# Optimization experiments

Hardware: AMD Instinct MI355X
Metric: run time of the kernel (lower is better)

## Reference

```python
import jax, jax.numpy as jnp
import numpy as np

N_NODES = 50000
N_EDGES = 800000
N_GRAPHS = 64
IN_CH = 128
HID = 128
PROC_X = 128
Q_DIM = 768
PROC_Q = 128
OUT_CH = 32


def setup_inputs() -> dict:
    key = jax.random.key(0)
    ks = jax.random.split(key, 16)
    inp = {
        "x": jax.random.normal(ks[0], (N_NODES, IN_CH), dtype=jnp.float32),
        "edge_index": jax.random.randint(ks[1], (2, N_EDGES), 0, N_NODES, dtype=jnp.int64),
        "batch": jnp.sort(jax.random.randint(ks[2], (N_NODES,), 0, N_GRAPHS, dtype=jnp.int64)),
        "question_embedding": jax.random.normal(ks[3], (N_GRAPHS, Q_DIM), dtype=jnp.float32),
    }
    s = 1.0 / np.sqrt(HID)
    inp["W0"] = jax.random.uniform(ks[4], (IN_CH, HID), minval=-s, maxval=s)
    inp["b0"] = jnp.zeros((HID,), jnp.float32)
    inp["W1"] = jax.random.uniform(ks[5], (HID, HID), minval=-s, maxval=s)
    inp["b1"] = jnp.zeros((HID,), jnp.float32)
    inp["W2"] = jax.random.uniform(ks[6], (HID, PROC_X), minval=-s, maxval=s)
    inp["b2"] = jnp.zeros((PROC_X,), jnp.float32)
    inp["fc0_w"] = jax.random.uniform(ks[7], (Q_DIM, PROC_Q), minval=-s, maxval=s)
    inp["fc0_b"] = jnp.zeros((PROC_Q,), jnp.float32)
    inp["fc1_w"] = jax.random.uniform(ks[8], (PROC_X + PROC_Q, HID), minval=-s, maxval=s)
    inp["fc1_b"] = jnp.zeros((HID,), jnp.float32)
    inp["fc2_w"] = jax.random.uniform(ks[9], (HID, OUT_CH), minval=-s, maxval=s)
    inp["fc2_b"] = jnp.zeros((OUT_CH,), jnp.float32)
    return inp


def _gcn_norm(edge_index, n_nodes):
    """Add self-loops and compute symmetric GCN normalization per edge."""
    loop = jnp.arange(n_nodes, dtype=edge_index.dtype)
    src = jnp.concatenate([edge_index[0], loop])
    dst = jnp.concatenate([edge_index[1], loop])
    ones = jnp.ones_like(dst, dtype=jnp.float32)
    deg = jax.ops.segment_sum(ones, dst, num_segments=n_nodes)
    dinv = jnp.where(deg > 0, jax.lax.rsqrt(deg), 0.0)
    norm = dinv[src] * dinv[dst]  # [E+N]
    return src, dst, norm


def _gcn_conv(x, src, dst, norm, W, b):
    h = x @ W                                # [N, F_out]
    msg = h[src] * norm[:, None]             # gather + scale  [E+N, F_out]
    agg = jax.ops.segment_sum(msg, dst, num_segments=x.shape[0])
    return agg + b


def reference(x, edge_index, batch, question_embedding,
              W0, b0, W1, b1, W2, b2,
              fc0_w, fc0_b, fc1_w, fc1_b, fc2_w, fc2_b):
    n = x.shape[0]
    src, dst, norm = _gcn_norm(edge_index, n)
    h = jax.nn.relu(_gcn_conv(x, src, dst, norm, W0, b0))
    h = jax.nn.relu(_gcn_conv(h, src, dst, norm, W1, b1))
    h = jax.nn.relu(_gcn_conv(h, src, dst, norm, W2, b2))
    q = jax.nn.relu(question_embedding @ fc0_w + fc0_b)  # [G, PROC_Q]
    q_exp = q[batch]                                      # [N, PROC_Q]
    combined = jnp.concatenate([h, q_exp], axis=1)
    out = jax.nn.relu(combined @ fc1_w + fc1_b)
    out = out @ fc2_w + fc2_b
    return out
```

## Files before the change

### kernel.cpp

```cpp
#include <hip/hip_runtime.h>
#include <hip/hip_bf16.h>

#define N_NODES 50000
#define N_EDGES 800000
#define N_GRAPHS 64
#define LSTR 136
#define NP 50016

typedef __attribute__((ext_vector_type(4))) short s4v;
typedef __attribute__((ext_vector_type(8))) short s8v;
typedef __attribute__((ext_vector_type(16))) float f16v;

struct HL { short hi, lo; };

__device__ inline HL bsplit(float f) {
    HL r;
    unsigned u = __float_as_uint(f);
    unsigned rh = (u + 0x7FFFu + ((u >> 16) & 1u)) >> 16;
    r.hi = (short)rh;
    float fh = __uint_as_float(rh << 16);
    float fl = f - fh;
    unsigned u2 = __float_as_uint(fl);
    unsigned rl = (u2 + 0x7FFFu + ((u2 >> 16) & 1u)) >> 16;
    r.lo = (short)rl;
    return r;
}

__device__ inline unsigned short f2bf(float f) {
    unsigned u = __float_as_uint(f);
    return (unsigned short)((u + 0x7FFFu + ((u >> 16) & 1u)) >> 16);
}

__device__ inline float bflo(unsigned u) { return __uint_as_float(u << 16); }
__device__ inline float bfhi(unsigned u) { return __uint_as_float(u & 0xFFFF0000u); }


__global__ __launch_bounds__(512) void k_scan_a(const int* __restrict__ cnt8,
                                                int* __restrict__ rowptr,
                                                int* __restrict__ bsum,
                                                float* __restrict__ dinv,
                                                int* __restrict__ base8, int n) {
    __shared__ int s[512];
    int t = threadIdx.x;
    int i = blockIdx.x * 512 + t;
    int deg = 0;
    if (i < n) {
        int b = 0;
        #pragma unroll
        for (int p = 0; p < 8; ++p) {
            int c = cnt8[p * NP + i];
            base8[p * NP + i] = b;
            b += c;
        }
        deg = b;
        dinv[i] = rsqrtf((float)(deg + 1));
    }
    int pv = (deg + 7) & ~7;
    s[t] = pv;
    __syncthreads();
    for (int d = 1; d < 512; d <<= 1) {
        int x = (t >= d) ? s[t - d] : 0;
        __syncthreads();
        s[t] += x;
        __syncthreads();
    }
    if (i < n) rowptr[i] = s[t] - pv;
    if (t == 511) bsum[blockIdx.x] = s[511];
}

__global__ __launch_bounds__(512) void k_scan_c(int* __restrict__ rowptr,
                                                const int* __restrict__ bsum,
                                                int n, int nb) {
    __shared__ int sb[128];
    int t = threadIdx.x;
    if (t < 128) sb[t] = (t < nb) ? bsum[t] : 0;
    __syncthreads();
    for (int d = 1; d < 128; d <<= 1) {
        int x = 0;
        if (t < 128 && t >= d) x = sb[t - d];
        __syncthreads();
        if (t < 128) sb[t] += x;
        __syncthreads();
    }
    int add = (blockIdx.x > 0) ? sb[blockIdx.x - 1] : 0;
    int i = blockIdx.x * 512 + t;
    if (i < n) rowptr[i] += add;
    if (i == 0) rowptr[n] = sb[nb - 1];
}

__global__ __launch_bounds__(512) void k_prep(const float* __restrict__ qe,
                                              const float* __restrict__ fc0w,
                                              const float* __restrict__ fc0b,
                                              const float* __restrict__ fc1w,
                                              const float* __restrict__ fc1b,
                                              const float* __restrict__ W0,
                                              const float* __restrict__ W1,
                                              const float* __restrict__ W2,
                                              const float* __restrict__ fc2w,
                                              const int* __restrict__ ei,
                                              int* __restrict__ cnt8,
                                              int* __restrict__ rank,
                                              short* __restrict__ WH,
                                              short* __restrict__ WL,
                                              unsigned* __restrict__ Hsd,
                                              unsigned short* __restrict__ colA,
                                              float* __restrict__ qq, int E) {
    int b = blockIdx.x, tid = threadIdx.x;
    if (b >= 482) {
        int e = (b - 482) * 512 + tid;
        if (e < E) {
            int dst = ei[E + e];
            int p = b & 7;
            int r = atomicAdd(&cnt8[p * NP + dst], 1);
            rank[e] = (p << 24) | r;
        }
        return;
    }
    if (b == 481) {
        if (tid < 64) Hsd[(unsigned)N_NODES * 64u + tid] = 0u;
        if (tid >= 64 && tid < 128) Hsd[100001u * 64u + (unsigned)(tid - 64)] = 0u;
        return;
    }
    if (b >= 200) {
        int idx = (b - 200) * 512 + tid;
        if (idx < 143752) {
            uint4 p;
            p.x = p.y = p.z = p.w = 0xC350C350u;
            ((uint4*)colA)[idx] = p;
        }
        return;
    }
    if (b >= 64) {
        int i = (b - 64) * 512 + tid;
        float val;
        int dst;
        if (i < 65536) {
            int mat = i >> 14, off = i & 16383;
            int k = off >> 7, n = off & 127;
            const float* src = (mat == 0) ? W0 : (mat == 1) ? W1 : (mat == 2) ? W2 : fc1w;
            val = src[k * 128 + n];
            dst = mat * 16384 + n * 128 + k;
        } else {
            int off = i - 65536;
            int k = off >> 5, n = off & 31;
            val = fc2w[k * 32 + n];
            dst = 65536 + n * 128 + k;
        }
        HL r = bsplit(val);
        WH[dst] = r.hi;
        WL[dst] = r.lo;
        return;
    }
    __shared__ float qs[768];
    __shared__ float red[512];
    __shared__ float ql[128];
    const float* fc1bot = fc1w + 128 * 128;
    int g = b;
    for (int i = tid; i < 768; i += 512) qs[i] = qe[g * 768 + i];
    __syncthreads();
    int j = tid & 127, sl = tid >> 7;
    int kb = sl * 192;
    float a0 = 0, a1 = 0, a2 = 0, a3 = 0;
    for (int k = 0; k < 192; k += 4) {
        a0 += qs[kb + k + 0] * fc0w[(kb + k + 0) * 128 + j];
        a1 += qs[kb + k + 1] * fc0w[(kb + k + 1) * 128 + j];
        a2 += qs[kb + k + 2] * fc0w[(kb + k + 2) * 128 + j];
        a3 += qs[kb + k + 3] * fc0w[(kb + k + 3) * 128 + j];
    }
    red[tid] = (a0 + a1) + (a2 + a3);
    __syncthreads();
    if (tid < 128)
        ql[tid] = fmaxf(((red[tid] + red[tid + 128]) + (red[tid + 256] + red[tid + 384]))
                        + fc0b[tid], 0.f);
    __syncthreads();
    kb = sl * 32;
    float b0 = 0, b1 = 0;
    for (int k = 0; k < 32; k += 2) {
        b0 += ql[kb + k + 0] * fc1bot[(kb + k + 0) * 128 + j];
        b1 += ql[kb + k + 1] * fc1bot[(kb + k + 1) * 128 + j];
    }
    red[tid] = b0 + b1;
    __syncthreads();
    if (tid < 128)
        qq[g * 128 + tid] = ((red[tid] + red[tid + 128]) + (red[tid + 256] + red[tid + 384]))
                            + fc1b[tid];
}

__global__ __launch_bounds__(128) void k_fg(const float* __restrict__ A32,
                                            const short* __restrict__ WTh,
                                            const short* __restrict__ WTl,
                                            const float* __restrict__ dinv,
                                            unsigned short* __restrict__ oHs,
                                            const int* __restrict__ ei,
                                            const int* __restrict__ rowptr,
                                            const int* __restrict__ rank,
                                            const int* __restrict__ base8,
                                            unsigned short* __restrict__ colA,
                                            int nrows, int E, int GG) {
    const int tid = threadIdx.x;
    if (blockIdx.x >= GG) {
        int e = (blockIdx.x - GG) * 128 + tid;
        if (e < E) {
            int dst = ei[E + e];
            int rk = rank[e];
            int p = rk >> 24, r = rk & 0xFFFFFF;
            colA[rowptr[dst] + base8[p * NP + dst] + r] = (unsigned short)ei[e];
        }
        return;
    }
    __shared__ short Ah[32 * LSTR];
    const int row0 = blockIdx.x * 32;

    #pragma unroll
    for (int i = 0; i < 8; ++i) {
        int u = i * 128 + tid;
        int r = u >> 5, c4 = u & 31;
        int gr = row0 + r;
        float4 v = make_float4(0.f, 0.f, 0.f, 0.f);
        if (gr < nrows) v = ((const float4*)A32)[(size_t)gr * 32 + c4];
        s4v h4 = {(short)f2bf(v.x), (short)f2bf(v.y), (short)f2bf(v.z), (short)f2bf(v.w)};
        *(s4v*)&Ah[r * LSTR + c4 * 4] = h4;
    }
    __syncthreads();

    const int wv = tid >> 6, lane = tid & 63;
    const int m = lane & 31, half = lane >> 5;
    const int c0 = wv * 64 + m;
    f16v acc0 = {0.f}, acc1 = {0.f};
    #pragma unroll
    for (int ks = 0; ks < 8; ++ks) {
        int ko = ks * 16 + half * 8;
        s8v ah  = *(const s8v*)&Ah[m * LSTR + ko];
        s8v bh0 = *(const s8v*)&WTh[(size_t)c0 * 128 + ko];
        s8v bl0 = *(const s8v*)&WTl[(size_t)c0 * 128 + ko];
        s8v bh1 = *(const s8v*)&WTh[(size_t)(c0 + 32) * 128 + ko];
        s8v bl1 = *(const s8v*)&WTl[(size_t)(c0 + 32) * 128 + ko];
        acc0 = __builtin_amdgcn_mfma_f32_32x32x16_bf16(ah, bh0, acc0, 0, 0, 0);
        acc0 = __builtin_amdgcn_mfma_f32_32x32x16_bf16(ah, bl0, acc0, 0, 0, 0);
        acc1 = __builtin_amdgcn_mfma_f32_32x32x16_bf16(ah, bh1, acc1, 0, 0, 0);
        acc1 = __builtin_amdgcn_mfma_f32_32x32x16_bf16(ah, bl1, acc1, 0, 0, 0);
    }

    #pragma unroll
    for (int reg = 0; reg < 16; ++reg) {
        int rl = (reg & 3) + 8 * (reg >> 2) + 4 * half;
        int gr = row0 + rl;
        if (gr >= nrows) continue;
        float sc = dinv[gr];
        oHs[(size_t)gr * 128 + c0]      = f2bf(acc0[reg] * sc);
        oHs[(size_t)gr * 128 + c0 + 32] = f2bf(acc1[reg] * sc);
    }
}

template <int FC>
__global__ __launch_bounds__(256, 7) void k_gg(const unsigned* __restrict__ Hs,
                                               const int* __restrict__ rowptr,
                                               const unsigned short* __restrict__ colA,
                                               const float* __restrict__ dinv,
                                               const float* __restrict__ bias,
                                               const short* __restrict__ WTh,
                                               const short* __restrict__ WTl,
                                               const short* __restrict__ W2h,
                                               const short* __restrict__ W2l,
                                               const float* __restrict__ qq,
                                               const int* __restrict__ batch,
                                               const float* __restrict__ fc2b,
                                               unsigned short* __restrict__ oHs,
                                               float* __restrict__ out,
                                               int n) {
    __shared__ short SM[(FC ? 64 : 32) * LSTR];
    short* Ah = SM;
    const int tid = threadIdx.x;
    const int row0 = blockIdx.x * 32;
    const int wv = tid >> 6, l = tid & 63;
    const int m = l & 31, half = l >> 5;
    const int il = l & 15;
    const unsigned ilo = (unsigned)(il * 4);
    const unsigned shq = (l & 16) ? 16u : 0u;
    const bool qhi = (l & 32) != 0;
    const bool q0 = (l < 16);

    int pidx = row0 + wv * 8 + l;
    if (pidx > N_NODES) pidx = N_NODES;
    const int rp = rowptr[pidx];
    const int dvu = (int)__float_as_uint(dinv[pidx < N_NODES ? pidx : N_NODES - 1]);

    const float4 bA = ((const float4*)bias)[il * 2];
    const float4 bB = ((const float4*)bias)[il * 2 + 1];

    int node = row0 + wv * 8;
    int e0 = __builtin_amdgcn_readfirstlane(__builtin_amdgcn_readlane(rp, 0));
    int e1 = __builtin_amdgcn_readfirstlane(__builtin_amdgcn_readlane(rp, 1));
    bool alive = node < n;
    bool act = alive && (e0 < e1);
    uint4 cwA = {0, 0, 0, 0}, sf = {0, 0, 0, 0};
    if (alive) sf = *(const uint4*)(Hs + (unsigned)node * 64u + ilo);
    if (act)   cwA = *(const uint4*)(colA + e0);

    for (int i = 0; i < 8; ++i) {
        float a0 = 0, a1 = 0, a2 = 0, a3 = 0, a4 = 0, a5 = 0, a6 = 0, a7 = 0;
        float c0f = 0, c1f = 0, c2f = 0, c3f = 0, c4f = 0, c5f = 0, c6f = 0, c7f = 0;
        if (act) {
            const int ng = (e1 - e0) >> 3;
            uint4 cwB = *(const uint4*)(colA + e0 + ((ng > 1) ? 8 : 0));
            int g = 0;
            while (g + 2 <= ng) {
                uint4 nA = *(const uint4*)(colA + e0 + ((g + 2 < ng) ? (g + 2) * 8 : 0));
                uint4 nB = *(const uint4*)(colA + e0 + ((g + 3 < ng) ? (g + 3) * 8 : 0));
                unsigned wAa = qhi ? cwA.y : cwA.x;
                unsigned wAb = qhi ? cwA.w : cwA.z;
                unsigned wBa = qhi ? cwB.y : cwB.x;
                unsigned wBb = qhi ? cwB.w : cwB.z;
                uint4 va = *(const uint4*)(Hs + ((wAa >> shq) & 0xFFFFu) * 64u + ilo);
                uint4 vb = *(const uint4*)(Hs + ((wAb >> shq) & 0xFFFFu) * 64u + ilo);
                uint4 vc = *(const uint4*)(Hs + ((wBa >> shq) & 0xFFFFu) * 64u + ilo);
                uint4 vd = *(const uint4*)(Hs + ((wBb >> shq) & 0xFFFFu) * 64u + ilo);
                a0 += bflo(va.x); a1 += bfhi(va.x);
                a2 += bflo(va.y); a3 += bfhi(va.y);
                a4 += bflo(va.z); a5 += bfhi(va.z);
                a6 += bflo(va.w); a7 += bfhi(va.w);
                c0f += bflo(vb.x); c1f += bfhi(vb.x);
                c2f += bflo(vb.y); c3f += bfhi(vb.y);
                c4f += bflo(vb.z); c5f += bfhi(vb.z);
                c6f += bflo(vb.w); c7f += bfhi(vb.w);
                a0 += bflo(vc.x); a1 += bfhi(vc.x);
                a2 += bflo(vc.y); a3 += bfhi(vc.y);
                a4 += bflo(vc.z); a5 += bfhi(vc.z);
                a6 += bflo(vc.w); a7 += bfhi(vc.w);
                c0f += bflo(vd.x); c1f += bfhi(vd.x);
                c2f += bflo(vd.y); c3f += bfhi(vd.y);
                c4f += bflo(vd.z); c5f += bfhi(vd.z);
                c6f += bflo(vd.w); c7f += bfhi(vd.w);
                cwA = nA; cwB = nB; g += 2;
            }
            if (g < ng) {
                unsigned wAa = qhi ? cwA.y : cwA.x;
                unsigned wAb = qhi ? cwA.w : cwA.z;
                uint4 va = *(const uint4*)(Hs + ((wAa >> shq) & 0xFFFFu) * 64u + ilo);
                uint4 vb = *(const uint4*)(Hs + ((wAb >> shq) & 0xFFFFu) * 64u + ilo);
                a0 += bflo(va.x); a1 += bfhi(va.x);
                a2 += bflo(va.y); a3 += bfhi(va.y);
                a4 += bflo(va.z); a5 += bfhi(va.z);
                a6 += bflo(va.w); a7 += bfhi(va.w);
                c0f += bflo(vb.x); c1f += bfhi(vb.x);
                c2f += bflo(vb.y); c3f += bfhi(vb.y);
                c4f += bflo(vb.z); c5f += bfhi(vb.z);
                c6f += bflo(vb.w); c7f += bfhi(vb.w);
            }
        }
        float s0 = a0 + c0f, s1 = a1 + c1f, s2 = a2 + c2f, s3 = a3 + c3f;
        float s4 = a4 + c4f, s5 = a5 + c5f, s6 = a6 + c6f, s7 = a7 + c7f;

        int e0n = e1;
        int e1n = (i < 7) ? __builtin_amdgcn_readfirstlane(__builtin_amdgcn_readlane(rp, i + 2)) : 0;
        int noden = node + 1;
        bool aliven = (i < 7) && (noden < n);
        bool actn = aliven && (e0n < e1n);
        uint4 cwn = {0, 0, 0, 0}, sfn = {0, 0, 0, 0};
        if (aliven) sfn = *(const uint4*)(Hs + (unsigned)noden * 64u + ilo);
        if (actn)   cwn = *(const uint4*)(colA + e0n);

        const int r = wv * 8 + i;
        if (alive) {
            s0 += __shfl_xor(s0, 16); s1 += __shfl_xor(s1, 16);
            s2 += __shfl_xor(s2, 16); s3 += __shfl_xor(s3, 16);
            s4 += __shfl_xor(s4, 16); s5 += __shfl_xor(s5, 16);
            s6 += __shfl_xor(s6, 16); s7 += __shfl_xor(s7, 16);
            s0 += __shfl_xor(s0, 32); s1 += __shfl_xor(s1, 32);
            s2 += __shfl_xor(s2, 32); s3 += __shfl_xor(s3, 32);
            s4 += __shfl_xor(s4, 32); s5 += __shfl_xor(s5, 32);
            s6 += __shfl_xor(s6, 32); s7 += __shfl_xor(s7, 32);
            float di = __uint_as_float((unsigned)__builtin_amdgcn_readlane(dvu, i));
            float o0 = fmaxf((s0 + bflo(sf.x)) * di + bA.x, 0.f);
            float o1 = fmaxf((s1 + bfhi(sf.x)) * di + bA.y, 0.f);
            float o2 = fmaxf((s2 + bflo(sf.y)) * di + bA.z, 0.f);
            float o3 = fmaxf((s3 + bfhi(sf.y)) * di + bA.w, 0.f);
            float o4 = fmaxf((s4 + bflo(sf.z)) * di + bB.x, 0.f);
            float o5 = fmaxf((s5 + bfhi(sf.z)) * di + bB.y, 0.f);
            float o6 = fmaxf((s6 + bflo(sf.w)) * di + bB.z, 0.f);
            float o7 = fmaxf((s7 + bfhi(sf.w)) * di + bB.w, 0.f);
            if (q0) {
                uint4 pk;
                pk.x = (unsigned)f2bf(o0) | ((unsigned)f2bf(o1) << 16);
                pk.y = (unsigned)f2bf(o2) | ((unsigned)f2bf(o3) << 16);
                pk.z = (unsigned)f2bf(o4) | ((unsigned)f2bf(o5) << 16);
                pk.w = (unsigned)f2bf(o6) | ((unsigned)f2bf(o7) << 16);
                *(uint4*)&Ah[r * LSTR + il * 8] = pk;
            }
        } else if (q0) {
            uint4 z = {0, 0, 0, 0};
            *(uint4*)&Ah[r * LSTR + il * 8] = z;
        }
        e0 = e0n; e1 = e1n; cwA = cwn; sf = sfn;
        act = actn; alive = aliven; node = noden;
    }
    __syncthreads();

    const int c0 = wv * 32 + m;
    f16v acc = {0.f};
    #pragma unroll
    for (int ks = 0; ks < 8; ++ks) {
        int ko = ks * 16 + half * 8;
        s8v ah = *(const s8v*)&Ah[m * LSTR + ko];
        s8v bh = *(const s8v*)&WTh[(size_t)c0 * 128 + ko];
        s8v bl = *(const s8v*)&WTl[(size_t)c0 * 128 + ko];
        acc = __builtin_amdgcn_mfma_f32_32x32x16_bf16(ah, bh, acc, 0, 0, 0);
        acc = __builtin_amdgcn_mfma_f32_32x32x16_bf16(ah, bl, acc, 0, 0, 0);
    }

    if (FC == 0) {
        #pragma unroll
        for (int reg = 0; reg < 16; ++reg) {
            int rl = (reg & 3) + 8 * (reg >> 2) + 4 * half;
            int gr = row0 + rl;
            if (gr >= n) continue;
            oHs[(size_t)gr * 128 + c0] = f2bf(acc[reg] * dinv[gr]);
        }
    } else {
        short* Pl = SM + 32 * LSTR;
        __syncthreads();
        #pragma unroll
        for (int reg = 0; reg < 16; ++reg) {
            int rl = (reg & 3) + 8 * (reg >> 2) + 4 * half;
            int gr = row0 + rl;
            int g = (gr < n) ? batch[gr] : 0;
            float v = fmaxf(acc[reg] + qq[(size_t)g * 128 + c0], 0.f);
            HL p = bsplit(v);
            Ah[rl * LSTR + c0] = p.hi;
            Pl[rl * LSTR + c0] = p.lo;
        }
        __syncthreads();
        f16v acc2 = {0.f};
        #pragma unroll
        for (int ks = 0; ks < 2; ++ks) {
            int ko = wv * 32 + ks * 16 + half * 8;
            s8v ah = *(const s8v*)&Ah[m * LSTR + ko];
            s8v al = *(const s8v*)&Pl[m * LSTR + ko];
            s8v bh = *(const s8v*)&W2h[(size_t)m * 128 + ko];
            s8v bl = *(const s8v*)&W2l[(size_t)m * 128 + ko];
            acc2 = __builtin_amdgcn_mfma_f32_32x32x16_bf16(ah, bh, acc2, 0, 0, 0);
            acc2 = __builtin_amdgcn_mfma_f32_32x32x16_bf16(ah, bl, acc2, 0, 0, 0);
            acc2 = __builtin_amdgcn_mfma_f32_32x32x16_bf16(al, bh, acc2, 0, 0, 0);
        }
        __syncthreads();
        float* red = (float*)SM;
        if (wv > 0) {
            #pragma unroll
            for (int reg = 0; reg < 16; ++reg) {
                int rl = (reg & 3) + 8 * (reg >> 2) + 4 * half;
                red[(wv - 1) * 1056 + rl * 33 + m] = acc2[reg];
            }
        }
        __syncthreads();
        if (wv == 0) {
            #pragma unroll
            for (int reg = 0; reg < 16; ++reg) {
                int rl = (reg & 3) + 8 * (reg >> 2) + 4 * half;
                int gr = row0 + rl;
                if (gr < n)
                    out[(size_t)gr * 32 + m] = acc2[reg]
                        + (red[rl * 33 + m] + red[1056 + rl * 33 + m])
                        + red[2112 + rl * 33 + m] + fc2b[m];
            }
        }
    }
}


extern "C" void kernel_launch(void* const* d_in, const int* in_sizes, int n_in,
                              void* d_out, int out_size, void* d_ws, size_t ws_size,
                              hipStream_t stream) {
    const float* x    = (const float*)d_in[0];
    const int*   ei   = (const int*)d_in[1];
    const int*   batch= (const int*)d_in[2];
    const float* qe   = (const float*)d_in[3];
    const float* W0   = (const float*)d_in[4];
    const float* b0   = (const float*)d_in[5];
    const float* W1   = (const float*)d_in[6];
    const float* b1   = (const float*)d_in[7];
    const float* W2   = (const float*)d_in[8];
    const float* b2   = (const float*)d_in[9];
    const float* fc0w = (const float*)d_in[10];
    const float* fc0b = (const float*)d_in[11];
    const float* fc1w = (const float*)d_in[12];
    const float* fc1b = (const float*)d_in[13];
    const float* fc2w = (const float*)d_in[14];
    const float* fc2b = (const float*)d_in[15];
    float* out = (float*)d_out;

    float* WS = (float*)d_ws;
    unsigned short* HS  = (unsigned short*)WS;
    unsigned short* HS2 = (unsigned short*)(WS + 3200064);
    float* DINV = WS + 6400128;
    float* QQ   = WS + 6450144;
    int*   ROWPTR = (int*)(WS + 6508352);
    int*   RANK = (int*)(WS + 6558368);
    unsigned short* COL = (unsigned short*)(WS + 7358368);
    int*   BSUM = (int*)(WS + 7933376);
    short* WTH  = (short*)(WS + 7933504);
    short* WTL  = WTH + 69632;
    int*   CNT8  = (int*)HS2;
    int*   BASE8 = CNT8 + 8 * NP;

    const int N = N_NODES, E = N_EDGES;
    const int sb = (N + 511) / 512;
    const int gg = (N + 31) / 32;
    const int histb = (E + 511) / 512;
    const int fillb = (E + 127) / 128;

    (void)hipMemsetAsync(CNT8, 0, 8 * NP * sizeof(int), stream);
    k_prep<<<482 + histb, 512, 0, stream>>>(qe, fc0w, fc0b, fc1w, fc1b,
                                            W0, W1, W2, fc2w, ei, CNT8, RANK,
                                            WTH, WTL, (unsigned*)HS, COL, QQ, E);
    k_scan_a<<<sb, 512, 0, stream>>>(CNT8, ROWPTR, BSUM, DINV, BASE8, N);
    k_scan_c<<<sb, 512, 0, stream>>>(ROWPTR, BSUM, N, sb);
    k_fg<<<gg + fillb, 128, 0, stream>>>(x, WTH, WTL, DINV, HS,
                                         ei, ROWPTR, RANK, BASE8, COL, N, E, gg);
    k_gg<0><<<gg, 256, 0, stream>>>((const unsigned*)HS, ROWPTR, COL, DINV, b0,
                                    WTH + 16384, WTL + 16384, nullptr, nullptr,
                                    nullptr, nullptr, nullptr, HS2, nullptr, N);
    k_gg<0><<<gg, 256, 0, stream>>>((const unsigned*)HS2, ROWPTR, COL, DINV, b1,
                                    WTH + 32768, WTL + 32768, nullptr, nullptr,
                                    nullptr, nullptr, nullptr, HS, nullptr, N);
    k_gg<1><<<gg, 256, 0, stream>>>((const unsigned*)HS, ROWPTR, COL, DINV, b2,
                                    WTH + 49152, WTL + 49152, WTH + 65536, WTL + 65536,
                                    QQ, batch, fc2b, nullptr, out, N);
}
```

Measured before the change: 305.2 us.

## Fuse two-pass prefix scan into single kernel with atomic cross-block handoff

Merges the block-local scan and the block-sum fixup into one kernel. The last block to finish scans all block totals and publishes each block's offset through atomic flags in workspace, while every block spins until its offset is ready. This removes one kernel launch and one rowptr read-modify-write pass. It also switches the bf16 hidden-state and output stores to nontemporal stores. The spin-wait relies on all 98 blocks being resident at the same time, which holds on this GPU but is a forward-progress risk in general.

```diff
diff --git a/kernel.cpp b/kernel.cpp
--- a/kernel.cpp
+++ b/kernel.cpp
@@ -34,25 +34,26 @@
 __device__ inline float bflo(unsigned u) { return __uint_as_float(u << 16); }
 __device__ inline float bfhi(unsigned u) { return __uint_as_float(u & 0xFFFF0000u); }
 
-
-__global__ __launch_bounds__(512) void k_scan_a(const int* __restrict__ cnt8,
-                                                int* __restrict__ rowptr,
-                                                int* __restrict__ bsum,
-                                                float* __restrict__ dinv,
-                                                int* __restrict__ base8, int n) {
+__global__ __launch_bounds__(512) void k_scan(const int* __restrict__ cnt8,
+                                              int* __restrict__ rowptr,
+                                              int* __restrict__ sync,
+                                              float* __restrict__ dinv,
+                                              int* __restrict__ base8, int n, int nb) {
     __shared__ int s[512];
-    int t = threadIdx.x;
-    int i = blockIdx.x * 512 + t;
+    __shared__ int s2[128];
+    __shared__ int flag;
+    const int t = threadIdx.x, b = blockIdx.x;
+    const int i = b * 512 + t;
     int deg = 0;
     if (i < n) {
-        int b = 0;
+        int acc = 0;
         #pragma unroll
         for (int p = 0; p < 8; ++p) {
             int c = cnt8[p * NP + i];
-            base8[p * NP + i] = b;
-            b += c;
-        }
-        deg = b;
+            base8[p * NP + i] = acc;
+            acc += c;
+        }
+        deg = acc;
         dinv[i] = rsqrtf((float)(deg + 1));
     }
     int pv = (deg + 7) & ~7;
@@ -64,28 +65,38 @@
         s[t] += x;
         __syncthreads();
     }
-    if (i < n) rowptr[i] = s[t] - pv;
-    if (t == 511) bsum[blockIdx.x] = s[511];
-}
-
-__global__ __launch_bounds__(512) void k_scan_c(int* __restrict__ rowptr,
-                                                const int* __restrict__ bsum,
-                                                int n, int nb) {
-    __shared__ int sb[128];
-    int t = threadIdx.x;
-    if (t < 128) sb[t] = (t < nb) ? bsum[t] : 0;
-    __syncthreads();
-    for (int d = 1; d < 128; d <<= 1) {
-        int x = 0;
-        if (t < 128 && t >= d) x = sb[t - d];
-        __syncthreads();
-        if (t < 128) sb[t] += x;
-        __syncthreads();
-    }
-    int add = (blockIdx.x > 0) ? sb[blockIdx.x - 1] : 0;
-    int i = blockIdx.x * 512 + t;
-    if (i < n) rowptr[i] += add;
-    if (i == 0) rowptr[n] = sb[nb - 1];
+    if (t == 0) {
+        atomicExch(&sync[b], s[511] + 1);
+        flag = (atomicAdd(&sync[128], 1) == nb - 1);
+    }
+    __syncthreads();
+    if (flag) {
+        int my = 0;
+        if (t < 128) {
+            int v = 0;
+            if (t < nb) { do { v = atomicAdd(&sync[t], 0); } while (v == 0); }
+            my = (v > 0) ? (v - 1) : 0;
+            s2[t] = my;
+        }
+        __syncthreads();
+        for (int d = 1; d < 128; d <<= 1) {
+            int x = 0;
+            if (t < 128 && t >= d) x = s2[t - d];
+            __syncthreads();
+            if (t < 128) s2[t] += x;
+            __syncthreads();
+        }
+        if (t < nb) atomicExch(&sync[160 + t], (s2[t] - my) + 1);
+    }
+    if (t == 0) {
+        int v;
+        do { v = atomicAdd(&sync[160 + b], 0); } while (v == 0);
+        flag = v - 1;
+    }
+    __syncthreads();
+    const int add = flag;
+    if (i < n) rowptr[i] = add + s[t] - pv;
+    if (b == nb - 1 && t == 511) rowptr[n] = add + s[511];
 }
 
 __global__ __launch_bounds__(512) void k_prep(const float* __restrict__ qe,
@@ -247,8 +258,8 @@
         int gr = row0 + rl;
         if (gr >= nrows) continue;
         float sc = dinv[gr];
-        oHs[(size_t)gr * 128 + c0]      = f2bf(acc0[reg] * sc);
-        oHs[(size_t)gr * 128 + c0 + 32] = f2bf(acc1[reg] * sc);
+        __builtin_nontemporal_store(f2bf(acc0[reg] * sc), &oHs[(size_t)gr * 128 + c0]);
+        __builtin_nontemporal_store(f2bf(acc1[reg] * sc), &oHs[(size_t)gr * 128 + c0 + 32]);
     }
 }
 
@@ -414,7 +425,8 @@
             int rl = (reg & 3) + 8 * (reg >> 2) + 4 * half;
             int gr = row0 + rl;
             if (gr >= n) continue;
-            oHs[(size_t)gr * 128 + c0] = f2bf(acc[reg] * dinv[gr]);
+            __builtin_nontemporal_store(f2bf(acc[reg] * dinv[gr]),
+                                        &oHs[(size_t)gr * 128 + c0]);
         }
     } else {
         short* Pl = SM + 32 * LSTR;
@@ -457,10 +469,12 @@
             for (int reg = 0; reg < 16; ++reg) {
                 int rl = (reg & 3) + 8 * (reg >> 2) + 4 * half;
                 int gr = row0 + rl;
-                if (gr < n)
-                    out[(size_t)gr * 32 + m] = acc2[reg]
+                if (gr < n) {
+                    float v = acc2[reg]
                         + (red[rl * 33 + m] + red[1056 + rl * 33 + m])
                         + red[2112 + rl * 33 + m] + fc2b[m];
+                    __builtin_nontemporal_store(v, &out[(size_t)gr * 32 + m]);
+                }
             }
         }
     }
@@ -496,11 +510,11 @@
     int*   ROWPTR = (int*)(WS + 6508352);
     int*   RANK = (int*)(WS + 6558368);
     unsigned short* COL = (unsigned short*)(WS + 7358368);
-    int*   BSUM = (int*)(WS + 7933376);
     short* WTH  = (short*)(WS + 7933504);
     short* WTL  = WTH + 69632;
     int*   CNT8  = (int*)HS2;
-    int*   BASE8 = CNT8 + 8 * NP;
+    int*   SYNC  = CNT8 + 8 * NP;
+    int*   BASE8 = SYNC + 320;
 
     const int N = N_NODES, E = N_EDGES;
     const int sb = (N + 511) / 512;
@@ -508,12 +522,11 @@
     const int histb = (E + 511) / 512;
     const int fillb = (E + 127) / 128;
 
-    (void)hipMemsetAsync(CNT8, 0, 8 * NP * sizeof(int), stream);
+    (void)hipMemsetAsync(CNT8, 0, (8 * NP + 320) * sizeof(int), stream);
     k_prep<<<482 + histb, 512, 0, stream>>>(qe, fc0w, fc0b, fc1w, fc1b,
                                             W0, W1, W2, fc2w, ei, CNT8, RANK,
                                             WTH, WTL, (unsigned*)HS, COL, QQ, E);
-    k_scan_a<<<sb, 512, 0, stream>>>(CNT8, ROWPTR, BSUM, DINV, BASE8, N);
-    k_scan_c<<<sb, 512, 0, stream>>>(ROWPTR, BSUM, N, sb);
+    k_scan<<<sb, 512, 0, stream>>>(CNT8, ROWPTR, SYNC, DINV, BASE8, N, sb);
     k_fg<<<gg + fillb, 128, 0, stream>>>(x, WTH, WTL, DINV, HS,
                                          ei, ROWPTR, RANK, BASE8, COL, N, E, gg);
     k_gg<0><<<gg, 256, 0, stream>>>((const unsigned*)HS, ROWPTR, COL, DINV, b0,
```

After: 307.9 us. Within noise of the previous version (+0.9%).
